# Optimization experiments

Hardware: AMD Instinct MI355X
Metric: run time of the kernel (lower is better)

The kernel has to match this reference:

```python
import jax, jax.numpy as jnp
import numpy as np

N_NODES = 50000
N_EDGES = 800000
IN_CH = 128
OUT_CH = 64
HID_CH = 2 * OUT_CH  # 128


def gcn_conv(x, edge_index, W, b, n_nodes):
    """PyG GCNConv: linear -> add self-loops -> sym-normalized scatter-add -> bias."""
    h = x @ W  # [N, out]
    loop = jnp.arange(n_nodes)
    row = jnp.concatenate([edge_index[0], loop])  # source nodes
    col = jnp.concatenate([edge_index[1], loop])  # target nodes
    deg = jax.ops.segment_sum(jnp.ones_like(col, dtype=h.dtype), col, num_segments=n_nodes)
    dinv = jnp.where(deg > 0, jax.lax.rsqrt(jnp.maximum(deg, 1.0)), 0.0)
    norm = dinv[row] * dinv[col]  # [E+N]
    msg = h[row] * norm[:, None]  # gather + scale, [E+N, out]
    out = jax.ops.segment_sum(msg, col, num_segments=n_nodes)  # scatter-add
    return out + b


def setup_inputs() -> dict:
    key = jax.random.key(0)
    ks = jax.random.split(key, 9)
    x = jax.random.normal(ks[0], (N_NODES, IN_CH), dtype=jnp.float32)
    edge_index = jax.random.randint(ks[1], (2, N_EDGES), 0, N_NODES, dtype=jnp.int64)
    s_in = 1.0 / np.sqrt(IN_CH)
    s_hid = 1.0 / np.sqrt(HID_CH)
    W1 = jax.random.normal(ks[2], (IN_CH, HID_CH), dtype=jnp.float32) * s_in
    b1 = jnp.zeros((HID_CH,), dtype=jnp.float32)
    W2 = jax.random.normal(ks[3], (HID_CH, OUT_CH), dtype=jnp.float32) * s_hid
    b2 = jnp.zeros((OUT_CH,), dtype=jnp.float32)
    W3 = jax.random.normal(ks[4], (HID_CH, OUT_CH), dtype=jnp.float32) * s_hid
    b3 = jnp.zeros((OUT_CH,), dtype=jnp.float32)
    return {"x": x, "edge_index": edge_index, "W1": W1, "b1": b1,
            "W2": W2, "b2": b2, "W3": W3, "b3": b3}


def reference(x, edge_index, W1, b1, W2, b2, W3, b3):
    act = jax.nn.relu
    hidden = act(gcn_conv(x, edge_index, W1, b1, N_NODES))
    x1 = act(gcn_conv(hidden, edge_index, W2, b2, N_NODES))
    x2 = act(gcn_conv(hidden, edge_index, W3, b3, N_NODES))
    return (x1, x2)
```

## Files before the change

kernel.cpp:

```cpp
#include <hip/hip_runtime.h>

#define N_NODES 50000
#define N_EDGES 800000
#define CH 128
#define WT_PAD 136
#define DUMMY N_NODES
#define SLOT_LOG 6
#define AGG_HALF_BLKS 1563

#define NBUCK 391
#define BUCK_CAP 3072
#define EPB 4096
#define PART_BLOCKS 196

typedef __attribute__((ext_vector_type(8))) short short8;
typedef __attribute__((ext_vector_type(4))) float floatx4;

__device__ __forceinline__ short f2bf(float f) {
    union { float f; unsigned u; } v; v.f = f;
    unsigned r = v.u + 0x7fff + ((v.u >> 16) & 1);
    return (short)(r >> 16);
}
__device__ __forceinline__ float bflo(unsigned u) {
    union { unsigned u; float f; } v; v.u = u << 16; return v.f;
}
__device__ __forceinline__ float bfhi(unsigned u) {
    union { unsigned u; float f; } v; v.u = u & 0xffff0000u; return v.f;
}


__global__ __launch_bounds__(256) void prep_kernel(const float* __restrict__ W1,
                                                   const float* __restrict__ W2,
                                                   const float* __restrict__ W3,
                                                   const float* __restrict__ b2,
                                                   const float* __restrict__ b3,
                                                   unsigned short* __restrict__ Wt1,
                                                   unsigned short* __restrict__ Wt23,
                                                   float* __restrict__ b23,
                                                   int* __restrict__ bucket_cnt,
                                                   unsigned int* __restrict__ gdummy) {
    int i = blockIdx.x * blockDim.x + threadIdx.x;
    if (i < 128 * 128) {
        int n = i >> 7, k = i & 127;
        Wt1[i] = (unsigned short)f2bf(W1[k * 128 + n]);
        float w = (n < 64) ? W2[k * 64 + n] : W3[k * 64 + (n - 64)];
        Wt23[i] = (unsigned short)f2bf(w);
    } else if (i < 128 * 128 + 128) {
        int k2 = i - 128 * 128;
        b23[k2] = (k2 < 64) ? b2[k2] : b3[k2 - 64];
    } else if (i < 128 * 128 + 192) {
        gdummy[i - (128 * 128 + 128)] = 0;
    }
    if (i < NBUCK) bucket_cnt[i] = 0;
}


__global__ __launch_bounds__(256) void partition(const int* __restrict__ ei,
                                                 int* __restrict__ bucket_cnt,
                                                 unsigned* __restrict__ bucket_data) {
    __shared__ int hcnt[512], hscan[512], htmp[512];
    __shared__ int s_shift[512];
    __shared__ unsigned stg[EPB];
    __shared__ int dsti[EPB];
    int tid = threadIdx.x;
    int e0 = blockIdx.x * EPB;

    for (int i = tid; i < 512; i += 256) hcnt[i] = 0;
    __syncthreads();
    for (int j = tid; j < EPB; j += 256) {
        int e = e0 + j;
        if (e < N_EDGES) atomicAdd(&hcnt[ei[N_EDGES + e] >> 7], 1);
    }
    __syncthreads();
    for (int i = tid; i < 512; i += 256) hscan[i] = hcnt[i];
    __syncthreads();
    for (int off = 1; off < 512; off <<= 1) {
        for (int i = tid; i < 512; i += 256) htmp[i] = hscan[i] + (i >= off ? hscan[i - off] : 0);
        __syncthreads();
        for (int i = tid; i < 512; i += 256) hscan[i] = htmp[i];
        __syncthreads();
    }
    for (int b = tid; b < NBUCK; b += 256) {
        int c = hcnt[b];
        int excl = hscan[b] - c;
        int g = (c > 0) ? atomicAdd(&bucket_cnt[b], c) : 0;
        s_shift[b] = g - excl;
        htmp[b] = excl;
    }
    __syncthreads();
    for (int j = tid; j < EPB; j += 256) {
        int e = e0 + j;
        if (e < N_EDGES) {
            int src = ei[e];
            int d = ei[N_EDGES + e];
            int b = d >> 7;
            int pos = atomicAdd(&htmp[b], 1);
            stg[pos] = ((unsigned)(d & 127) << 16) | (unsigned)src;
            int gidx = s_shift[b] + pos;
            dsti[pos] = (gidx < BUCK_CAP) ? (b * BUCK_CAP + gidx) : -1;
        }
    }
    __syncthreads();
    int tot = N_EDGES - e0; if (tot > EPB) tot = EPB;
    for (int j = tid; j < tot; j += 256) {
        int di = dsti[j];
        if (di >= 0) bucket_data[di] = stg[j];
    }
}


__global__ __launch_bounds__(256) void csr_build(const unsigned* __restrict__ bucket_data,
                                                 const int* __restrict__ bucket_cnt,
                                                 int* __restrict__ counts,
                                                 unsigned short* __restrict__ sorted_src) {
    __shared__ uint4 slots4[1024];
    __shared__ int ctr[128];
    unsigned short* slots = (unsigned short*)slots4;
    int tid = threadIdx.x, b = blockIdx.x;

    for (int i = tid; i < 128; i += 256) ctr[i] = 0;
    const unsigned dpat = ((unsigned)DUMMY) | (((unsigned)DUMMY) << 16);
    for (int i = tid; i < 1024; i += 256) slots4[i] = make_uint4(dpat, dpat, dpat, dpat);
    __syncthreads();

    int cnt = bucket_cnt[b]; if (cnt > BUCK_CAP) cnt = BUCK_CAP;
    const unsigned* bd = bucket_data + b * BUCK_CAP;
    for (int j = tid; j < cnt; j += 256) {
        unsigned w = bd[j];
        int dl = (int)(w >> 16);
        int r = atomicAdd(&ctr[dl], 1);
        if (r < 64) slots[(dl << 6) + r] = (unsigned short)(w & 0xffffu);
    }
    __syncthreads();

    int node0 = b << 7;
    for (int i = tid; i < 128; i += 256)
        if (node0 + i < N_NODES) counts[node0 + i] = ctr[i];
    uint4* gs = (uint4*)(sorted_src + ((size_t)node0 << SLOT_LOG));
    for (int k = tid; k < 1024; k += 256) {
        int row = k >> 3;
        if (node0 + row < N_NODES) gs[k] = slots4[k];
    }
}


template <bool A_BF16>
__global__ __launch_bounds__(256) void gemm_mfma(const void* __restrict__ Ain,
                                                 const unsigned short* __restrict__ Wt,
                                                 const int* __restrict__ degs,
                                                 unsigned short* __restrict__ g) {
    __shared__ unsigned short lds[128 * WT_PAD];
    int tid = threadIdx.x;
    int wave = tid >> 6, lane = tid & 63;
    int quad = lane >> 4, ln = lane & 15;

    {
        int r = tid >> 1, h = tid & 1;
        const int4* src = (const int4*)(Wt + r * 128 + h * 64);
#pragma unroll
        for (int i = 0; i < 8; ++i)
            *(int4*)&lds[r * WT_PAD + h * 64 + i * 8] = src[i];
    }

    int row_base = blockIdx.x * 64 + wave * 16;
    int arow = row_base + ln;
    bool ok = arow < N_NODES;
    short8 afrag[4];
    if (A_BF16) {
        const unsigned short* A = (const unsigned short*)Ain;
#pragma unroll
        for (int kk = 0; kk < 4; ++kk) {
            short8 v = {};
            if (ok) v = *(const short8*)(A + arow * 128 + kk * 32 + quad * 8);
            afrag[kk] = v;
        }
    } else {
        const float* A = (const float*)Ain;
#pragma unroll
        for (int kk = 0; kk < 4; ++kk) {
            short8 v = {};
            if (ok) {
                const floatx4* p = (const floatx4*)(A + arow * 128 + kk * 32 + quad * 8);
                floatx4 fa = p[0], fb = p[1];
                v[0] = f2bf(fa.x); v[1] = f2bf(fa.y); v[2] = f2bf(fa.z); v[3] = f2bf(fa.w);
                v[4] = f2bf(fb.x); v[5] = f2bf(fb.y); v[6] = f2bf(fb.z); v[7] = f2bf(fb.w);
            }
            afrag[kk] = v;
        }
    }
    __syncthreads();

    floatx4 acc[8] = {};
#pragma unroll
    for (int n0 = 0; n0 < 8; ++n0) {
#pragma unroll
        for (int kk = 0; kk < 4; ++kk) {
            short8 b = *(const short8*)&lds[(n0 * 16 + ln) * WT_PAD + kk * 32 + quad * 8];
            acc[n0] = __builtin_amdgcn_mfma_f32_16x16x32_bf16(afrag[kk], b, acc[n0], 0, 0, 0);
        }
    }

    __syncthreads();
    unsigned short* st = &lds[wave * 16 * WT_PAD];
    float dv[4];
#pragma unroll
    for (int r = 0; r < 4; ++r) {
        int node = row_base + quad * 4 + r;
        dv[r] = (node < N_NODES) ? rsqrtf((float)(degs[node] + 1)) : 0.f;
    }
#pragma unroll
    for (int n0 = 0; n0 < 8; ++n0)
#pragma unroll
        for (int r = 0; r < 4; ++r)
            st[(quad * 4 + r) * WT_PAD + n0 * 16 + ln] =
                (unsigned short)f2bf(acc[n0][r] * dv[r]);
    __syncthreads();

#pragma unroll
    for (int i = 0; i < 4; ++i) {
        int row = i * 4 + quad;
        int node = row_base + row;
        short8 v = *(const short8*)&st[row * WT_PAD + ln * 8];
        if (node < N_NODES) *(short8*)(g + node * 128 + ln * 8) = v;
    }
}


template <int MODE>
__global__ __launch_bounds__(256) void aggregate_bf16(const unsigned short* __restrict__ g,
                                                      const int* __restrict__ degs,
                                                      const unsigned short* __restrict__ srcs,
                                                      const float* __restrict__ bias,
                                                      void* __restrict__ outp) {
    int h = 0, nb = blockIdx.x;
    if (nb >= AGG_HALF_BLKS) { h = 1; nb -= AGG_HALF_BLKS; }
    int n = nb * 32 + (threadIdx.x >> 3);
    if (n >= N_NODES) return;
    int c4 = threadIdx.x & 7;
    int hoff = h * 8;
    const uint4* grow = (const uint4*)g;
    uint4 u = grow[n * 16 + hoff + c4];
    float a0 = bflo(u.x), a1 = bfhi(u.x), a2 = bflo(u.y), a3 = bfhi(u.y);
    float a4 = bflo(u.z), a5 = bfhi(u.z), a6 = bflo(u.w), a7 = bfhi(u.w);
    float c0 = 0.f, c1 = 0.f, c2 = 0.f, c3 = 0.f, c5 = 0.f, c6 = 0.f, c7 = 0.f, c8 = 0.f;
    int deg = degs[n];
    int degc = deg > 64 ? 64 : deg;
    int beg = n << SLOT_LOG;
    int pend = beg + ((degc + 3) & ~3);
    int e = beg;
    for (; e + 8 <= pend; e += 8) {
        ushort4 sa = *(const ushort4*)&srcs[e];
        ushort4 sb = *(const ushort4*)&srcs[e + 4];
        uint4 v0 = grow[sa.x * 16 + hoff + c4];
        uint4 v1 = grow[sa.y * 16 + hoff + c4];
        uint4 v2 = grow[sa.z * 16 + hoff + c4];
        uint4 v3 = grow[sa.w * 16 + hoff + c4];
        uint4 v4 = grow[sb.x * 16 + hoff + c4];
        uint4 v5 = grow[sb.y * 16 + hoff + c4];
        uint4 v6 = grow[sb.z * 16 + hoff + c4];
        uint4 v7 = grow[sb.w * 16 + hoff + c4];
        a0 += bflo(v0.x); a1 += bfhi(v0.x); a2 += bflo(v0.y); a3 += bfhi(v0.y);
        a4 += bflo(v0.z); a5 += bfhi(v0.z); a6 += bflo(v0.w); a7 += bfhi(v0.w);
        c0 += bflo(v1.x); c1 += bfhi(v1.x); c2 += bflo(v1.y); c3 += bfhi(v1.y);
        c5 += bflo(v1.z); c6 += bfhi(v1.z); c7 += bflo(v1.w); c8 += bfhi(v1.w);
        a0 += bflo(v2.x); a1 += bfhi(v2.x); a2 += bflo(v2.y); a3 += bfhi(v2.y);
        a4 += bflo(v2.z); a5 += bfhi(v2.z); a6 += bflo(v2.w); a7 += bfhi(v2.w);
        c0 += bflo(v3.x); c1 += bfhi(v3.x); c2 += bflo(v3.y); c3 += bfhi(v3.y);
        c5 += bflo(v3.z); c6 += bfhi(v3.z); c7 += bflo(v3.w); c8 += bfhi(v3.w);
        a0 += bflo(v4.x); a1 += bfhi(v4.x); a2 += bflo(v4.y); a3 += bfhi(v4.y);
        a4 += bflo(v4.z); a5 += bfhi(v4.z); a6 += bflo(v4.w); a7 += bfhi(v4.w);
        c0 += bflo(v5.x); c1 += bfhi(v5.x); c2 += bflo(v5.y); c3 += bfhi(v5.y);
        c5 += bflo(v5.z); c6 += bfhi(v5.z); c7 += bflo(v5.w); c8 += bfhi(v5.w);
        a0 += bflo(v6.x); a1 += bfhi(v6.x); a2 += bflo(v6.y); a3 += bfhi(v6.y);
        a4 += bflo(v6.z); a5 += bfhi(v6.z); a6 += bflo(v6.w); a7 += bfhi(v6.w);
        c0 += bflo(v7.x); c1 += bfhi(v7.x); c2 += bflo(v7.y); c3 += bfhi(v7.y);
        c5 += bflo(v7.z); c6 += bfhi(v7.z); c7 += bflo(v7.w); c8 += bfhi(v7.w);
    }
    if (e < pend) {
        ushort4 sa = *(const ushort4*)&srcs[e];
        uint4 v0 = grow[sa.x * 16 + hoff + c4];
        uint4 v1 = grow[sa.y * 16 + hoff + c4];
        uint4 v2 = grow[sa.z * 16 + hoff + c4];
        uint4 v3 = grow[sa.w * 16 + hoff + c4];
        a0 += bflo(v0.x); a1 += bfhi(v0.x); a2 += bflo(v0.y); a3 += bfhi(v0.y);
        a4 += bflo(v0.z); a5 += bfhi(v0.z); a6 += bflo(v0.w); a7 += bfhi(v0.w);
        c0 += bflo(v1.x); c1 += bfhi(v1.x); c2 += bflo(v1.y); c3 += bfhi(v1.y);
        c5 += bflo(v1.z); c6 += bfhi(v1.z); c7 += bflo(v1.w); c8 += bfhi(v1.w);
        a0 += bflo(v2.x); a1 += bfhi(v2.x); a2 += bflo(v2.y); a3 += bfhi(v2.y);
        a4 += bflo(v2.z); a5 += bfhi(v2.z); a6 += bflo(v2.w); a7 += bfhi(v2.w);
        c0 += bflo(v3.x); c1 += bfhi(v3.x); c2 += bflo(v3.y); c3 += bfhi(v3.y);
        c5 += bflo(v3.z); c6 += bfhi(v3.z); c7 += bflo(v3.w); c8 += bfhi(v3.w);
    }
    a0 += c0; a1 += c1; a2 += c2; a3 += c3; a4 += c5; a5 += c6; a6 += c7; a7 += c8;
    float d = rsqrtf((float)(deg + 1));
    float4 bv0 = ((const float4*)bias)[h * 16 + c4 * 2];
    float4 bv1 = ((const float4*)bias)[h * 16 + c4 * 2 + 1];
    float o0 = fmaxf(d * a0 + bv0.x, 0.f);
    float o1 = fmaxf(d * a1 + bv0.y, 0.f);
    float o2 = fmaxf(d * a2 + bv0.z, 0.f);
    float o3 = fmaxf(d * a3 + bv0.w, 0.f);
    float o4 = fmaxf(d * a4 + bv1.x, 0.f);
    float o5 = fmaxf(d * a5 + bv1.y, 0.f);
    float o6 = fmaxf(d * a6 + bv1.z, 0.f);
    float o7 = fmaxf(d * a7 + bv1.w, 0.f);
    if (MODE == 0) {
        uint4 w;
        w.x = ((unsigned)(unsigned short)f2bf(o0)) | (((unsigned)(unsigned short)f2bf(o1)) << 16);
        w.y = ((unsigned)(unsigned short)f2bf(o2)) | (((unsigned)(unsigned short)f2bf(o3)) << 16);
        w.z = ((unsigned)(unsigned short)f2bf(o4)) | (((unsigned)(unsigned short)f2bf(o5)) << 16);
        w.w = ((unsigned)(unsigned short)f2bf(o6)) | (((unsigned)(unsigned short)f2bf(o7)) << 16);
        ((uint4*)outp)[n * 16 + hoff + c4] = w;
    } else {
        float* out = (float*)outp + (size_t)h * N_NODES * 64;
        floatx4* o = (floatx4*)out + n * 16 + c4 * 2;
        floatx4 w0; w0.x = o0; w0.y = o1; w0.z = o2; w0.w = o3;
        floatx4 w1; w1.x = o4; w1.y = o5; w1.z = o6; w1.w = o7;
        __builtin_nontemporal_store(w0, o);
        __builtin_nontemporal_store(w1, o + 1);
    }
}


extern "C" void kernel_launch(void* const* d_in, const int* in_sizes, int n_in,
                              void* d_out, int out_size, void* d_ws, size_t ws_size,
                              hipStream_t stream) {
    const float* x  = (const float*)d_in[0];
    const int*   ei = (const int*)d_in[1];
    const float* W1 = (const float*)d_in[2];
    const float* b1 = (const float*)d_in[3];
    const float* W2 = (const float*)d_in[4];
    const float* b2 = (const float*)d_in[5];
    const float* W3 = (const float*)d_in[6];
    const float* b3 = (const float*)d_in[7];
    float* out = (float*)d_out;

    char* w = (char*)d_ws;
    int*            counts      = (int*)(w + 0);
    int*            bucket_cnt  = (int*)(w + 200704);
    unsigned short* Wt1         = (unsigned short*)(w + 204800);
    unsigned short* Wt23        = (unsigned short*)(w + 237568);
    float*          b23         = (float*)(w + 270336);
    unsigned*       bucket_data = (unsigned*)(w + 278528);
    unsigned short* sorted_src  = (unsigned short*)(w + 5083136);
    unsigned short* g1          = (unsigned short*)(w + 11483136);
    unsigned short* hidden      = (unsigned short*)(w + 24283392);

    prep_kernel<<<66, 256, 0, stream>>>(W1, W2, W3, b2, b3, Wt1, Wt23, b23, bucket_cnt,
                                        (unsigned int*)(g1 + N_NODES * 128));
    partition<<<PART_BLOCKS, 256, 0, stream>>>(ei, bucket_cnt, bucket_data);
    csr_build<<<NBUCK, 256, 0, stream>>>(bucket_data, bucket_cnt, counts, sorted_src);

    const int gemm_blocks = (N_NODES + 63) / 64;
    const int agg_blocks = 2 * AGG_HALF_BLKS;

    gemm_mfma<false><<<gemm_blocks, 256, 0, stream>>>(x, Wt1, counts, g1);
    aggregate_bf16<0><<<agg_blocks, 256, 0, stream>>>(g1, counts, sorted_src, b1, hidden);

    gemm_mfma<true><<<gemm_blocks, 256, 0, stream>>>(hidden, Wt23, counts, g1);
    aggregate_bf16<1><<<agg_blocks, 256, 0, stream>>>(g1, counts, sorted_src, b23, out);
}
```

Before: 190.9 us.

## Sort nodes by degree within each bucket to balance aggregate wavefront work

csr_build now bitonic-sorts the 128 nodes of each bucket by in-degree and writes a permutation plus sorted counts, reordering the slot rows to match. The aggregate kernels process nodes in this sorted order, so nodes with similar degree share a wavefront and the per-wave loop trip count is more uniform. This cuts divergence-induced idle lanes, but adds a sort in csr_build, an extra perm load per thread, and scattered output stores.

```diff
diff --git a/kernel.cpp b/kernel.cpp
--- a/kernel.cpp
+++ b/kernel.cpp
@@ -6,7 +6,8 @@
 #define WT_PAD 136
 #define DUMMY N_NODES
 #define SLOT_LOG 6
-#define AGG_HALF_BLKS 1563
+#define NPOS (391 * 128)
+#define AGG_HALF_BLKS 1564
 
 #define NBUCK 391
 #define BUCK_CAP 3072
@@ -112,9 +113,12 @@
 __global__ __launch_bounds__(256) void csr_build(const unsigned* __restrict__ bucket_data,
                                                  const int* __restrict__ bucket_cnt,
                                                  int* __restrict__ counts,
+                                                 int* __restrict__ perm,
+                                                 int* __restrict__ counts_s,
                                                  unsigned short* __restrict__ sorted_src) {
     __shared__ uint4 slots4[1024];
     __shared__ int ctr[128];
+    __shared__ int key[128];
     unsigned short* slots = (unsigned short*)slots4;
     int tid = threadIdx.x, b = blockIdx.x;
 
@@ -136,10 +140,37 @@
     int node0 = b << 7;
     for (int i = tid; i < 128; i += 256)
         if (node0 + i < N_NODES) counts[node0 + i] = ctr[i];
+    if (tid < 128) {
+        int d = (node0 + tid < N_NODES) ? ctr[tid] : (1 << 13);
+        key[tid] = (d << 16) | tid;
+    }
+    __syncthreads();
+    for (int k = 2; k <= 128; k <<= 1) {
+        for (int j = k >> 1; j > 0; j >>= 1) {
+            if (tid < 128) {
+                int ixj = tid ^ j;
+                if (ixj > tid) {
+                    int a = key[tid], c = key[ixj];
+                    bool asc = ((tid & k) == 0);
+                    if (asc ? (a > c) : (a < c)) { key[tid] = c; key[ixj] = a; }
+                }
+            }
+            __syncthreads();
+        }
+    }
+    if (tid < 128) {
+        int li = key[tid] & 0xffff;
+        int node = node0 + li;
+        bool valid = node < N_NODES;
+        perm[node0 + tid] = valid ? node : -1;
+        counts_s[node0 + tid] = valid ? ctr[li] : 0;
+    }
+    __syncthreads();
     uint4* gs = (uint4*)(sorted_src + ((size_t)node0 << SLOT_LOG));
-    for (int k = tid; k < 1024; k += 256) {
-        int row = k >> 3;
-        if (node0 + row < N_NODES) gs[k] = slots4[k];
+    for (int k2 = tid; k2 < 1024; k2 += 256) {
+        int row = k2 >> 3;
+        int li = key[row] & 0xffff;
+        gs[k2] = slots4[(li << 3) + (k2 & 7)];
     }
 }
 
@@ -228,22 +259,24 @@
 
 template <int MODE>
 __global__ __launch_bounds__(256) void aggregate_bf16(const unsigned short* __restrict__ g,
-                                                      const int* __restrict__ degs,
+                                                      const int* __restrict__ perm,
+                                                      const int* __restrict__ counts_s,
                                                       const unsigned short* __restrict__ srcs,
                                                       const float* __restrict__ bias,
                                                       void* __restrict__ outp) {
     int h = 0, nb = blockIdx.x;
     if (nb >= AGG_HALF_BLKS) { h = 1; nb -= AGG_HALF_BLKS; }
     int n = nb * 32 + (threadIdx.x >> 3);
-    if (n >= N_NODES) return;
+    int pn = perm[n];
+    if (pn < 0) return;
     int c4 = threadIdx.x & 7;
     int hoff = h * 8;
     const uint4* grow = (const uint4*)g;
-    uint4 u = grow[n * 16 + hoff + c4];
+    uint4 u = grow[pn * 16 + hoff + c4];
     float a0 = bflo(u.x), a1 = bfhi(u.x), a2 = bflo(u.y), a3 = bfhi(u.y);
     float a4 = bflo(u.z), a5 = bfhi(u.z), a6 = bflo(u.w), a7 = bfhi(u.w);
     float c0 = 0.f, c1 = 0.f, c2 = 0.f, c3 = 0.f, c5 = 0.f, c6 = 0.f, c7 = 0.f, c8 = 0.f;
-    int deg = degs[n];
+    int deg = counts_s[n];
     int degc = deg > 64 ? 64 : deg;
     int beg = n << SLOT_LOG;
     int pend = beg + ((degc + 3) & ~3);
@@ -309,10 +342,10 @@
         w.y = ((unsigned)(unsigned short)f2bf(o2)) | (((unsigned)(unsigned short)f2bf(o3)) << 16);
         w.z = ((unsigned)(unsigned short)f2bf(o4)) | (((unsigned)(unsigned short)f2bf(o5)) << 16);
         w.w = ((unsigned)(unsigned short)f2bf(o6)) | (((unsigned)(unsigned short)f2bf(o7)) << 16);
-        ((uint4*)outp)[n * 16 + hoff + c4] = w;
+        ((uint4*)outp)[pn * 16 + hoff + c4] = w;
     } else {
         float* out = (float*)outp + (size_t)h * N_NODES * 64;
-        floatx4* o = (floatx4*)out + n * 16 + c4 * 2;
+        floatx4* o = (floatx4*)out + pn * 16 + c4 * 2;
         floatx4 w0; w0.x = o0; w0.y = o1; w0.z = o2; w0.w = o3;
         floatx4 w1; w1.x = o4; w1.y = o5; w1.z = o6; w1.w = o7;
         __builtin_nontemporal_store(w0, o);
@@ -337,25 +370,30 @@
     char* w = (char*)d_ws;
     int*            counts      = (int*)(w + 0);
     int*            bucket_cnt  = (int*)(w + 200704);
-    unsigned short* Wt1         = (unsigned short*)(w + 204800);
-    unsigned short* Wt23        = (unsigned short*)(w + 237568);
-    float*          b23         = (float*)(w + 270336);
-    unsigned*       bucket_data = (unsigned*)(w + 278528);
-    unsigned short* sorted_src  = (unsigned short*)(w + 5083136);
-    unsigned short* g1          = (unsigned short*)(w + 11483136);
-    unsigned short* hidden      = (unsigned short*)(w + 24283392);
+    int*            perm        = (int*)(w + 204800);
+    int*            counts_s    = (int*)(w + 405504);
+    unsigned short* Wt1         = (unsigned short*)(w + 606208);
+    unsigned short* Wt23        = (unsigned short*)(w + 638976);
+    float*          b23         = (float*)(w + 671744);
+    unsigned*       bucket_data = (unsigned*)(w + 673792);
+    unsigned short* sorted_src  = (unsigned short*)(w + 5478400);
+    unsigned short* g1          = (unsigned short*)(w + 11884544);
+    unsigned short* hidden      = (unsigned short*)(w + 24684800);
 
     prep_kernel<<<66, 256, 0, stream>>>(W1, W2, W3, b2, b3, Wt1, Wt23, b23, bucket_cnt,
                                         (unsigned int*)(g1 + N_NODES * 128));
     partition<<<PART_BLOCKS, 256, 0, stream>>>(ei, bucket_cnt, bucket_data);
-    csr_build<<<NBUCK, 256, 0, stream>>>(bucket_data, bucket_cnt, counts, sorted_src);
+    csr_build<<<NBUCK, 256, 0, stream>>>(bucket_data, bucket_cnt, counts, perm, counts_s,
+                                         sorted_src);
 
     const int gemm_blocks = (N_NODES + 63) / 64;
     const int agg_blocks = 2 * AGG_HALF_BLKS;
 
     gemm_mfma<false><<<gemm_blocks, 256, 0, stream>>>(x, Wt1, counts, g1);
-    aggregate_bf16<0><<<agg_blocks, 256, 0, stream>>>(g1, counts, sorted_src, b1, hidden);
+    aggregate_bf16<0><<<agg_blocks, 256, 0, stream>>>(g1, perm, counts_s, sorted_src, b1,
+                                                      hidden);
 
     gemm_mfma<true><<<gemm_blocks, 256, 0, stream>>>(hidden, Wt23, counts, g1);
-    aggregate_bf16<1><<<agg_blocks, 256, 0, stream>>>(g1, counts, sorted_src, b23, out);
-}
+    aggregate_bf16<1><<<agg_blocks, 256, 0, stream>>>(g1, perm, counts_s, sorted_src, b23,
+                                                      out);
+}
```

Result: slower. 197.4 us (+3.4%).

## Fuse all GCN stages into one cooperative persistent kernel with grid syncs

Applied to the files above, without the earlier changes.

Merges the seven separate launches (prep, partition, CSR build, two GEMMs, two aggregations) into a single cooperative kernel. Blocks loop over virtual block ids in each phase, with grid.sync between phases, and share one static LDS buffer. The partition phase also drops its per-edge destination-index array: it packs the full destination into the staged word and recomputes the bucket at scatter time. This is meant to remove launch gaps and inter-kernel tails. In exchange it adds grid-wide barrier cost, and the largest per-phase LDS demand may cap occupancy for the memory-bound aggregation phases.

```diff
diff --git a/kernel.cpp b/kernel.cpp
--- a/kernel.cpp
+++ b/kernel.cpp
@@ -1,8 +1,10 @@
 #include <hip/hip_runtime.h>
+#include <hip/hip_cooperative_groups.h>
+
+namespace cg = cooperative_groups;
 
 #define N_NODES 50000
 #define N_EDGES 800000
-#define CH 128
 #define WT_PAD 136
 #define DUMMY N_NODES
 #define SLOT_LOG 6
@@ -12,6 +14,9 @@
 #define BUCK_CAP 3072
 #define EPB 4096
 #define PART_BLOCKS 196
+#define GEMM_BLOCKS 782
+#define PREP_BLOCKS 66
+#define SMEM_BYTES 34816
 
 typedef __attribute__((ext_vector_type(8))) short short8;
 typedef __attribute__((ext_vector_type(4))) float floatx4;
@@ -29,17 +34,17 @@
 }
 
 
-__global__ __launch_bounds__(256) void prep_kernel(const float* __restrict__ W1,
-                                                   const float* __restrict__ W2,
-                                                   const float* __restrict__ W3,
-                                                   const float* __restrict__ b2,
-                                                   const float* __restrict__ b3,
-                                                   unsigned short* __restrict__ Wt1,
-                                                   unsigned short* __restrict__ Wt23,
-                                                   float* __restrict__ b23,
-                                                   int* __restrict__ bucket_cnt,
-                                                   unsigned int* __restrict__ gdummy) {
-    int i = blockIdx.x * blockDim.x + threadIdx.x;
+__device__ __forceinline__ void phase_prep(const float* __restrict__ W1,
+                                           const float* __restrict__ W2,
+                                           const float* __restrict__ W3,
+                                           const float* __restrict__ b2,
+                                           const float* __restrict__ b3,
+                                           unsigned short* __restrict__ Wt1,
+                                           unsigned short* __restrict__ Wt23,
+                                           float* __restrict__ b23,
+                                           int* __restrict__ bucket_cnt,
+                                           unsigned int* __restrict__ gdummy, int vb) {
+    int i = vb * 256 + threadIdx.x;
     if (i < 128 * 128) {
         int n = i >> 7, k = i & 127;
         Wt1[i] = (unsigned short)f2bf(W1[k * 128 + n]);
@@ -55,15 +60,16 @@
 }
 
 
-__global__ __launch_bounds__(256) void partition(const int* __restrict__ ei,
-                                                 int* __restrict__ bucket_cnt,
-                                                 unsigned* __restrict__ bucket_data) {
-    __shared__ int hcnt[512], hscan[512], htmp[512];
-    __shared__ int s_shift[512];
-    __shared__ unsigned stg[EPB];
-    __shared__ int dsti[EPB];
+__device__ __forceinline__ void phase_partition(char* smem, const int* __restrict__ ei,
+                                                int* __restrict__ bucket_cnt,
+                                                unsigned* __restrict__ bucket_data, int vb) {
+    int* hcnt    = (int*)smem;
+    int* hscan   = hcnt + 512;
+    int* htmp    = hscan + 512;
+    int* s_shift = htmp + 512;
+    unsigned* stg = (unsigned*)(s_shift + 512);
     int tid = threadIdx.x;
-    int e0 = blockIdx.x * EPB;
+    int e0 = vb * EPB;
 
     for (int i = tid; i < 512; i += 256) hcnt[i] = 0;
     __syncthreads();
@@ -83,8 +89,8 @@
     for (int b = tid; b < NBUCK; b += 256) {
         int c = hcnt[b];
         int excl = hscan[b] - c;
-        int g = (c > 0) ? atomicAdd(&bucket_cnt[b], c) : 0;
-        s_shift[b] = g - excl;
+        int gg = (c > 0) ? atomicAdd(&bucket_cnt[b], c) : 0;
+        s_shift[b] = gg - excl;
         htmp[b] = excl;
     }
     __syncthreads();
@@ -93,30 +99,30 @@
         if (e < N_EDGES) {
             int src = ei[e];
             int d = ei[N_EDGES + e];
-            int b = d >> 7;
-            int pos = atomicAdd(&htmp[b], 1);
-            stg[pos] = ((unsigned)(d & 127) << 16) | (unsigned)src;
-            int gidx = s_shift[b] + pos;
-            dsti[pos] = (gidx < BUCK_CAP) ? (b * BUCK_CAP + gidx) : -1;
+            int pos = atomicAdd(&htmp[d >> 7], 1);
+            stg[pos] = ((unsigned)d << 16) | (unsigned)src;
         }
     }
     __syncthreads();
     int tot = N_EDGES - e0; if (tot > EPB) tot = EPB;
     for (int j = tid; j < tot; j += 256) {
-        int di = dsti[j];
-        if (di >= 0) bucket_data[di] = stg[j];
-    }
-}
-
-
-__global__ __launch_bounds__(256) void csr_build(const unsigned* __restrict__ bucket_data,
-                                                 const int* __restrict__ bucket_cnt,
-                                                 int* __restrict__ counts,
-                                                 unsigned short* __restrict__ sorted_src) {
-    __shared__ uint4 slots4[1024];
-    __shared__ int ctr[128];
+        unsigned wv = stg[j];
+        int b = (int)(wv >> 23);
+        int gidx = s_shift[b] + j;
+        if (gidx < BUCK_CAP) bucket_data[b * BUCK_CAP + gidx] = wv;
+    }
+    __syncthreads();
+}
+
+
+__device__ __forceinline__ void phase_csr(char* smem, const unsigned* __restrict__ bucket_data,
+                                          const int* __restrict__ bucket_cnt,
+                                          int* __restrict__ counts,
+                                          unsigned short* __restrict__ sorted_src, int b) {
+    uint4* slots4 = (uint4*)smem;
+    int* ctr = (int*)(smem + 16384);
     unsigned short* slots = (unsigned short*)slots4;
-    int tid = threadIdx.x, b = blockIdx.x;
+    int tid = threadIdx.x;
 
     for (int i = tid; i < 128; i += 256) ctr[i] = 0;
     const unsigned dpat = ((unsigned)DUMMY) | (((unsigned)DUMMY) << 16);
@@ -126,10 +132,10 @@
     int cnt = bucket_cnt[b]; if (cnt > BUCK_CAP) cnt = BUCK_CAP;
     const unsigned* bd = bucket_data + b * BUCK_CAP;
     for (int j = tid; j < cnt; j += 256) {
-        unsigned w = bd[j];
-        int dl = (int)(w >> 16);
+        unsigned w2 = bd[j];
+        int dl = (int)((w2 >> 16) & 127);
         int r = atomicAdd(&ctr[dl], 1);
-        if (r < 64) slots[(dl << 6) + r] = (unsigned short)(w & 0xffffu);
+        if (r < 64) slots[(dl << 6) + r] = (unsigned short)(w2 & 0xffffu);
     }
     __syncthreads();
 
@@ -141,15 +147,16 @@
         int row = k >> 3;
         if (node0 + row < N_NODES) gs[k] = slots4[k];
     }
+    __syncthreads();
 }
 
 
 template <bool A_BF16>
-__global__ __launch_bounds__(256) void gemm_mfma(const void* __restrict__ Ain,
-                                                 const unsigned short* __restrict__ Wt,
-                                                 const int* __restrict__ degs,
-                                                 unsigned short* __restrict__ g) {
-    __shared__ unsigned short lds[128 * WT_PAD];
+__device__ __forceinline__ void phase_gemm(char* smem, const void* __restrict__ Ain,
+                                           const unsigned short* __restrict__ Wt,
+                                           const int* __restrict__ degs,
+                                           unsigned short* __restrict__ g, int vb) {
+    unsigned short* lds = (unsigned short*)smem;
     int tid = threadIdx.x;
     int wave = tid >> 6, lane = tid & 63;
     int quad = lane >> 4, ln = lane & 15;
@@ -162,7 +169,7 @@
             *(int4*)&lds[r * WT_PAD + h * 64 + i * 8] = src[i];
     }
 
-    int row_base = blockIdx.x * 64 + wave * 16;
+    int row_base = vb * 64 + wave * 16;
     int arow = row_base + ln;
     bool ok = arow < N_NODES;
     short8 afrag[4];
@@ -223,16 +230,17 @@
         short8 v = *(const short8*)&st[row * WT_PAD + ln * 8];
         if (node < N_NODES) *(short8*)(g + node * 128 + ln * 8) = v;
     }
+    __syncthreads();
 }
 
 
 template <int MODE>
-__global__ __launch_bounds__(256) void aggregate_bf16(const unsigned short* __restrict__ g,
-                                                      const int* __restrict__ degs,
-                                                      const unsigned short* __restrict__ srcs,
-                                                      const float* __restrict__ bias,
-                                                      void* __restrict__ outp) {
-    int h = 0, nb = blockIdx.x;
+__device__ __forceinline__ void phase_agg(const unsigned short* __restrict__ g,
+                                          const int* __restrict__ degs,
+                                          const unsigned short* __restrict__ srcs,
+                                          const float* __restrict__ bias,
+                                          void* __restrict__ outp, int vb) {
+    int h = 0, nb = vb;
     if (nb >= AGG_HALF_BLKS) { h = 1; nb -= AGG_HALF_BLKS; }
     int n = nb * 32 + (threadIdx.x >> 3);
     if (n >= N_NODES) return;
@@ -321,6 +329,48 @@
 }
 
 
+__global__ __launch_bounds__(256, 4) void mega(const float* __restrict__ x,
+                                               const int* __restrict__ ei,
+                                               const float* __restrict__ W1,
+                                               const float* __restrict__ b1,
+                                               const float* __restrict__ W2,
+                                               const float* __restrict__ b2,
+                                               const float* __restrict__ W3,
+                                               const float* __restrict__ b3,
+                                               float* __restrict__ out,
+                                               int* counts, int* bucket_cnt,
+                                               unsigned short* Wt1, unsigned short* Wt23,
+                                               float* b23, unsigned* bucket_data,
+                                               unsigned short* sorted_src,
+                                               unsigned short* g1, unsigned short* hidden) {
+    __shared__ __align__(16) char smem[SMEM_BYTES];
+    cg::grid_group grid = cg::this_grid();
+    int bid = blockIdx.x, gsz = gridDim.x;
+
+    for (int vb = bid; vb < PREP_BLOCKS; vb += gsz)
+        phase_prep(W1, W2, W3, b2, b3, Wt1, Wt23, b23, bucket_cnt,
+                   (unsigned int*)(g1 + N_NODES * 128), vb);
+    grid.sync();
+    for (int vb = bid; vb < PART_BLOCKS; vb += gsz)
+        phase_partition(smem, ei, bucket_cnt, bucket_data, vb);
+    grid.sync();
+    for (int vb = bid; vb < NBUCK; vb += gsz)
+        phase_csr(smem, bucket_data, bucket_cnt, counts, sorted_src, vb);
+    grid.sync();
+    for (int vb = bid; vb < GEMM_BLOCKS; vb += gsz)
+        phase_gemm<false>(smem, x, Wt1, counts, g1, vb);
+    grid.sync();
+    for (int vb = bid; vb < 2 * AGG_HALF_BLKS; vb += gsz)
+        phase_agg<0>(g1, counts, sorted_src, b1, hidden, vb);
+    grid.sync();
+    for (int vb = bid; vb < GEMM_BLOCKS; vb += gsz)
+        phase_gemm<true>(smem, hidden, Wt23, counts, g1, vb);
+    grid.sync();
+    for (int vb = bid; vb < 2 * AGG_HALF_BLKS; vb += gsz)
+        phase_agg<1>(g1, counts, sorted_src, b23, out, vb);
+}
+
+
 extern "C" void kernel_launch(void* const* d_in, const int* in_sizes, int n_in,
                               void* d_out, int out_size, void* d_ws, size_t ws_size,
                               hipStream_t stream) {
@@ -345,17 +395,22 @@
     unsigned short* g1          = (unsigned short*)(w + 11483136);
     unsigned short* hidden      = (unsigned short*)(w + 24283392);
 
-    prep_kernel<<<66, 256, 0, stream>>>(W1, W2, W3, b2, b3, Wt1, Wt23, b23, bucket_cnt,
-                                        (unsigned int*)(g1 + N_NODES * 128));
-    partition<<<PART_BLOCKS, 256, 0, stream>>>(ei, bucket_cnt, bucket_data);
-    csr_build<<<NBUCK, 256, 0, stream>>>(bucket_data, bucket_cnt, counts, sorted_src);
-
-    const int gemm_blocks = (N_NODES + 63) / 64;
-    const int agg_blocks = 2 * AGG_HALF_BLKS;
-
-    gemm_mfma<false><<<gemm_blocks, 256, 0, stream>>>(x, Wt1, counts, g1);
-    aggregate_bf16<0><<<agg_blocks, 256, 0, stream>>>(g1, counts, sorted_src, b1, hidden);
-
-    gemm_mfma<true><<<gemm_blocks, 256, 0, stream>>>(hidden, Wt23, counts, g1);
-    aggregate_bf16<1><<<agg_blocks, 256, 0, stream>>>(g1, counts, sorted_src, b23, out);
-}
+    static int coop_grid = 0;
+    if (coop_grid == 0) {
+        int nb = 0;
+        hipError_t e1 = hipOccupancyMaxActiveBlocksPerMultiprocessor(
+            &nb, reinterpret_cast<const void*>(mega), 256, 0);
+        int dev = 0, ncu = 0;
+        hipGetDevice(&dev);
+        hipError_t e2 = hipDeviceGetAttribute(&ncu, hipDeviceAttributeMultiprocessorCount, dev);
+        coop_grid = (e1 == hipSuccess && e2 == hipSuccess && nb > 0 && ncu > 0) ? nb * ncu : 512;
+        if (coop_grid > 2 * AGG_HALF_BLKS) coop_grid = 2 * AGG_HALF_BLKS;
+    }
+
+    void* args[] = {(void*)&x, (void*)&ei, (void*)&W1, (void*)&b1, (void*)&W2, (void*)&b2,
+                    (void*)&W3, (void*)&b3, (void*)&out, (void*)&counts, (void*)&bucket_cnt,
+                    (void*)&Wt1, (void*)&Wt23, (void*)&b23, (void*)&bucket_data,
+                    (void*)&sorted_src, (void*)&g1, (void*)&hidden};
+    hipLaunchCooperativeKernel(reinterpret_cast<const void*>(mega), dim3(coop_grid),
+                               dim3(256), args, 0, stream);
+}
```

New measurement: 570.4 us. 2.99x slower.
